# Kernel tuning notes

Hardware: AMD Instinct MI355X
Metric: run time of the kernel (lower is better)

## Reference

```python
import jax, jax.numpy as jnp
import numpy as np

# --- Mamba2Enc config (matches init_kwargs + mamba_ssm Mamba2 defaults) ---
D_IN = 1024
D_MODEL = 512
N_CLASSES = 2
NLAYERS = 2
D_STATE = 64
D_CONV = 4
EXPAND = 2
HEADDIM = 64
D_INNER = EXPAND * D_MODEL            # 1024
NHEADS = D_INNER // HEADDIM           # 16
CONV_DIM = D_INNER + 2 * D_STATE      # 1152 (ngroups=1)
D_IN_PROJ = 2 * D_INNER + 2 * D_STATE + NHEADS  # 2192
EPS = 1e-5


def setup_inputs() -> dict:
    key = jax.random.key(0)
    ks = jax.random.split(key, 10)
    def w(k, shape, sc=0.02):
        return jax.random.normal(k, shape, jnp.float32) * sc
    x = jax.random.normal(ks[0], (4, 4096, D_IN), jnp.float32)
    # fc1
    W1 = w(ks[1], (D_MODEL, D_IN))
    b1 = jnp.zeros((D_MODEL,), jnp.float32)
    # per-layer params stacked on leading NLAYERS axis
    ln_w = jnp.ones((NLAYERS, D_MODEL), jnp.float32)
    ln_b = jnp.zeros((NLAYERS, D_MODEL), jnp.float32)
    W_in = w(ks[2], (NLAYERS, D_IN_PROJ, D_MODEL))
    conv_w = w(ks[3], (NLAYERS, CONV_DIM, D_CONV), 0.1)
    conv_b = jnp.zeros((NLAYERS, CONV_DIM), jnp.float32)
    # dt_bias so that softplus(dt_bias) ~ [0.001, 0.1] (mamba init range)
    dt_bias = jax.random.uniform(ks[4], (NLAYERS, NHEADS), jnp.float32, -6.0, -2.3)
    A_log = jnp.log(jnp.tile(jnp.arange(1, NHEADS + 1, dtype=jnp.float32), (NLAYERS, 1)))
    Dskip = jnp.ones((NLAYERS, NHEADS), jnp.float32)
    norm_w = jnp.ones((NLAYERS, D_INNER), jnp.float32)
    W_out = w(ks[5], (NLAYERS, D_MODEL, D_INNER))
    # classifier
    Wc = w(ks[6], (N_CLASSES, D_MODEL))
    bc = jnp.zeros((N_CLASSES,), jnp.float32)
    return dict(x=x, W1=W1, b1=b1, ln_w=ln_w, ln_b=ln_b, W_in=W_in,
                conv_w=conv_w, conv_b=conv_b, dt_bias=dt_bias, A_log=A_log,
                Dskip=Dskip, norm_w=norm_w, W_out=W_out, Wc=Wc, bc=bc)


def _layernorm(h, w, b):
    mu = jnp.mean(h, axis=-1, keepdims=True)
    var = jnp.mean(jnp.square(h - mu), axis=-1, keepdims=True)
    return (h - mu) * jax.lax.rsqrt(var + EPS) * w + b


def _silu(x):
    return x * jax.nn.sigmoid(x)


def _mamba2(x, W_in, conv_w, conv_b, dt_bias, A_log, Dskip, norm_w, W_out):
    b, l, _ = x.shape
    zxbcdt = jnp.einsum('bld,ed->ble', x, W_in)  # (b, l, D_IN_PROJ)
    z = zxbcdt[..., :D_INNER]
    xBC = zxbcdt[..., D_INNER:D_INNER + CONV_DIM]
    dt = jax.nn.softplus(zxbcdt[..., -NHEADS:] + dt_bias)  # (b, l, h)
    # causal depthwise conv1d (kernel D_CONV) + silu
    xp = jnp.pad(xBC, ((0, 0), (D_CONV - 1, 0), (0, 0)))
    xBC = sum(xp[:, k:k + l, :] * conv_w[:, k] for k in range(D_CONV)) + conv_b
    xBC = _silu(xBC)
    xh = xBC[..., :D_INNER].reshape(b, l, NHEADS, HEADDIM)
    B = xBC[..., D_INNER:D_INNER + D_STATE]   # (b, l, n) ngroups=1
    C = xBC[..., D_INNER + D_STATE:]          # (b, l, n)
    A = -jnp.exp(A_log)                       # (h,)
    dA = jnp.exp(dt * A)                      # (b, l, h)
    dtx = dt[..., None] * xh                  # (b, l, h, p)

    def step(hstate, inp):
        dA_t, dtx_t, B_t, C_t = inp  # (b,h), (b,h,p), (b,n), (b,n)
        hstate = hstate * dA_t[:, :, None, None] + dtx_t[:, :, None, :] * B_t[:, None, :, None]
        y = jnp.einsum('bn,bhnp->bhp', C_t, hstate)
        return hstate, y

    init = jnp.zeros((b, NHEADS, D_STATE, HEADDIM), x.dtype)
    xs = (dA.transpose(1, 0, 2), dtx.transpose(1, 0, 2, 3),
          B.transpose(1, 0, 2), C.transpose(1, 0, 2))
    _, ys = jax.lax.scan(step, init, xs)      # ys: (l, b, h, p)
    y = ys.transpose(1, 0, 2, 3) + Dskip[None, None, :, None] * xh
    y = y.reshape(b, l, D_INNER)
    # RMSNormGated (norm_before_gate=False): rmsnorm(y * silu(z)) * weight
    y = y * _silu(z)
    y = y * jax.lax.rsqrt(jnp.mean(jnp.square(y), axis=-1, keepdims=True) + EPS) * norm_w
    return jnp.einsum('ble,de->bld', y, W_out)


def reference(x, W1, b1, ln_w, ln_b, W_in, conv_w, conv_b, dt_bias, A_log,
              Dskip, norm_w, W_out, Wc, bc):
    # fc1: Linear + GELU (dropout is identity at eval)
    h = jax.nn.gelu(jnp.einsum('bli,di->bld', x, W1) + b1, approximate=False)
    for i in range(NLAYERS):
        h = h + _mamba2(_layernorm(h, ln_w[i], ln_b[i]), W_in[i], conv_w[i],
                        conv_b[i], dt_bias[i], A_log[i], Dskip[i], norm_w[i], W_out[i])
    return jnp.einsum('bld,cd->blc', h, Wc) + bc
```

## Files before the change

kernel.cpp:

```cpp
#include <hip/hip_runtime.h>
#include <hip/hip_bf16.h>
#include <math.h>

#define BATCH 4
#define SEQ 4096
#define ROWS 16384
#define DIN 1024
#define DMODEL 512
#define DINNER 1024
#define DSTATE 64
#define NH 16
#define HD 64
#define CONVDIM 1152
#define DPROJ 2192
#define NPAD 2304
#define QC 64
#define NCH 64
#define LD 72

typedef __attribute__((ext_vector_type(8))) __bf16 bf16x8;
typedef __attribute__((ext_vector_type(4))) __bf16 bf16x4;
typedef __attribute__((ext_vector_type(4))) float f32x4;

__device__ __forceinline__ float siluf(float x){ return x / (1.f + __expf(-x)); }
__device__ __forceinline__ float geluf(float x){ return 0.5f*x*(1.f + erff(x*0.70710678118654752440f)); }

__device__ __forceinline__ bf16x8 scale8(bf16x8 v, float s){
  bf16x8 r;
  #pragma unroll
  for (int e = 0; e < 8; e++) r[e] = (__bf16)((float)v[e]*s);
  return r;
}

__device__ __forceinline__ void gl_lds16(const void* g, void* l){
  __builtin_amdgcn_global_load_lds((const __attribute__((address_space(1))) void*)g,
                                   (__attribute__((address_space(3))) void*)l, 16, 0, 0);
}

__global__ void cast_bf16_kernel(const float* __restrict__ src, __bf16* __restrict__ dst, long n){
  long i = (long)blockIdx.x*blockDim.x + threadIdx.x;
  long stride = (long)gridDim.x*blockDim.x;
  for (; i < n; i += stride) dst[i] = (__bf16)src[i];
}

__global__ void pad_win_kernel(const float* __restrict__ src, __bf16* __restrict__ dst){
  long total = 2L*NPAD*DMODEL;
  long i = (long)blockIdx.x*blockDim.x + threadIdx.x;
  long stride = (long)gridDim.x*blockDim.x;
  for (; i < total; i += stride){
    int k = (int)(i % DMODEL);
    int n = (int)((i / DMODEL) % NPAD);
    int l = (int)(i / ((long)DMODEL*NPAD));
    float v = (n < DPROJ) ? src[((long)l*DPROJ + n)*DMODEL + k] : 0.f;
    dst[i] = (__bf16)v;
  }
}

template<typename OutT, int EPI, int BM, int BN>
__global__ __launch_bounds__(256) void gemm_bt(const __bf16* __restrict__ A, const __bf16* __restrict__ Bm,
                                               OutT* __restrict__ C, const float* __restrict__ bias,
                                               int K, int Nc){
  constexpr int MI = BM/32, NI = BN/32;
  constexpr int CHA = BM/64;
  constexpr int CHT = (BM+BN)/64;
  __shared__ __align__(16) __bf16 As[2][BM*32];
  __shared__ __align__(16) __bf16 Bs[2][BN*32];
  int bm = blockIdx.x, bn = blockIdx.y;
  int tid = threadIdx.x;
  int lane = tid & 63, wid = tid >> 6;
  int wm = (wid >> 1)*(BM/2), wn = (wid & 1)*(BN/2);
  int lr = lane & 15, kb = lane >> 4;
  f32x4 acc[MI][NI] = {};
  const char* Ab = (const char*)A + (size_t)bm*BM*(size_t)(K*2);
  const char* Bb = (const char*)Bm + (size_t)bn*BN*(size_t)(K*2);
  int nkk = K >> 5;

  auto STAGE = [&](int kk, int buf){
    #pragma unroll
    for (int it = 0; it < CHT; it++){
      int cbase = it*4096 + wid*1024;
      int off = cbase + lane*16;
      int row = off >> 6, cb = off & 63;
      if (it < CHA) gl_lds16(Ab + (size_t)row*(K*2) + kk*64 + cb, (char*)(&As[buf][0]) + cbase);
      else          gl_lds16(Bb + (size_t)(row - BM)*(K*2) + kk*64 + cb, (char*)(&Bs[buf][0]) + (cbase - BM*64));
    }
  };

  STAGE(0, 0);
  for (int kk = 0; kk < nkk; kk++){
    int cur = kk & 1;
    if (kk + 1 < nkk){
      STAGE(kk + 1, cur ^ 1);
      asm volatile("s_waitcnt vmcnt(%0)" :: "n"(CHT) : "memory");
    } else {
      asm volatile("s_waitcnt vmcnt(0)" ::: "memory");
    }
    __builtin_amdgcn_sched_barrier(0);
    __builtin_amdgcn_s_barrier();
    __builtin_amdgcn_sched_barrier(0);
    const __bf16* Asb = &As[cur][0];
    const __bf16* Bsb = &Bs[cur][0];
    bf16x8 af[MI], bfr[NI];
    #pragma unroll
    for (int mi = 0; mi < MI; mi++) af[mi] = *(const bf16x8*)(Asb + (wm + mi*16 + lr)*32 + kb*8);
    #pragma unroll
    for (int ni = 0; ni < NI; ni++) bfr[ni] = *(const bf16x8*)(Bsb + (wn + ni*16 + lr)*32 + kb*8);
    #pragma unroll
    for (int mi = 0; mi < MI; mi++)
      #pragma unroll
      for (int ni = 0; ni < NI; ni++)
        acc[mi][ni] = __builtin_amdgcn_mfma_f32_16x16x32_bf16(af[mi], bfr[ni], acc[mi][ni], 0, 0, 0);
    __builtin_amdgcn_s_barrier();
    __builtin_amdgcn_sched_barrier(0);
  }
  #pragma unroll
  for (int mi = 0; mi < MI; mi++){
    #pragma unroll
    for (int ni = 0; ni < NI; ni++){
      int r0 = bm*BM + wm + mi*16 + (lane >> 4)*4;
      int c  = bn*BN + wn + ni*16 + lr;
      if (c < Nc){
        OutT* Cp = C + (size_t)r0*Nc + c;
        #pragma unroll
        for (int j = 0; j < 4; j++){
          float v = acc[mi][ni][j];
          if (EPI == 1){ float u = v + bias[c]; v = geluf(u); }
          if (EPI == 2){ v += (float)Cp[(size_t)j*Nc]; }
          Cp[(size_t)j*Nc] = (OutT)v;
        }
      }
    }
  }
}

__global__ __launch_bounds__(256) void ln_kernel(const float* __restrict__ h, const float* __restrict__ w,
                                                 const float* __restrict__ b, __bf16* __restrict__ out){
  int row = blockIdx.x*4 + (threadIdx.x >> 6);
  int lane = threadIdx.x & 63;
  const float* hr = h + (size_t)row*DMODEL + lane*8;
  float4 a = *(const float4*)hr, a2 = *(const float4*)(hr+4);
  float v[8] = {a.x,a.y,a.z,a.w,a2.x,a2.y,a2.z,a2.w};
  float s = 0.f;
  #pragma unroll
  for (int i = 0; i < 8; i++) s += v[i];
  #pragma unroll
  for (int o = 32; o; o >>= 1) s += __shfl_xor(s, o, 64);
  float mu = s*(1.f/512.f);
  float q = 0.f;
  #pragma unroll
  for (int i = 0; i < 8; i++){ float d = v[i]-mu; q += d*d; }
  #pragma unroll
  for (int o = 32; o; o >>= 1) q += __shfl_xor(q, o, 64);
  float rs = rsqrtf(q*(1.f/512.f) + 1e-5f);
  const float* wp = w + lane*8; const float* bp = b + lane*8;
  bf16x8 o8;
  #pragma unroll
  for (int i = 0; i < 8; i++) o8[i] = (__bf16)((v[i]-mu)*rs*wp[i] + bp[i]);
  *(bf16x8*)(out + (size_t)row*DMODEL + lane*8) = o8;
}

__global__ __launch_bounds__(256) void conv_bc(const __bf16* __restrict__ zx, const float* __restrict__ cw,
                                               const float* __restrict__ cb, __bf16* __restrict__ BCc){
  int idx = blockIdx.x*256 + threadIdx.x;
  int j = idx & 127;
  long bt = idx >> 7;
  int t = (int)(bt & (SEQ-1));
  int ch = DINNER + j;
  const __bf16* src = zx + (size_t)bt*DPROJ + 2048 + j;
  float acc = cb[ch] + (float)src[0]*cw[ch*4+3];
  if (t >= 1) acc += (float)src[-1L*DPROJ]*cw[ch*4+2];
  if (t >= 2) acc += (float)src[-2L*DPROJ]*cw[ch*4+1];
  if (t >= 3) acc += (float)src[-3L*DPROJ]*cw[ch*4+0];
  BCc[idx] = (__bf16)siluf(acc);
}

__global__ __launch_bounds__(256) void dt_kernel(const __bf16* __restrict__ zx, const float* __restrict__ dt_bias,
                                                 float* __restrict__ dtT){
  int idx = blockIdx.x*256 + threadIdx.x;
  int hh = idx & (NH-1); long bt = idx >> 4;
  int b = (int)(bt >> 12); int t = (int)(bt & (SEQ-1));
  float v = (float)zx[(size_t)bt*DPROJ + (DPROJ-NH) + hh] + dt_bias[hh];
  float sp = (v > 20.f) ? v : log1pf(__expf(v));
  dtT[((size_t)b*NH + hh)*SEQ + t] = sp;
}

__global__ __launch_bounds__(128) void ssd_state(const __bf16* __restrict__ zx, const __bf16* __restrict__ BCc,
                                                 const float* __restrict__ dtT, const float* __restrict__ A_log,
                                                 const float* __restrict__ cw, const float* __restrict__ cb,
                                                 __bf16* __restrict__ Schunk, float* __restrict__ Pbuf,
                                                 __bf16* __restrict__ xhT){
  __shared__ __align__(16) __bf16 Bt_all[2][64*LD];
  __shared__ __align__(16) __bf16 Xt_all[2][64*LD];
  int widx = threadIdx.x >> 6, lane = threadIdx.x & 63;
  int c = blockIdx.x*2 + widx, h = blockIdx.y, b = blockIdx.z;
  __bf16* Bt = Bt_all[widx];
  __bf16* Xt = Xt_all[widx];
  int lr = lane & 15, kb = lane >> 4, hi4 = lane >> 4;
  long t0 = (long)c*QC;
  size_t bt0 = (size_t)b*SEQ + t0;
  int bh = b*NH + h;
  float Ac = -expf(A_log[h]);
  float dtv = dtT[(size_t)bh*SEQ + t0 + lane];
  float cum = dtv*Ac;
  #pragma unroll
  for (int off = 1; off < 64; off <<= 1){ float v = __shfl_up(cum, off, 64); if (lane >= off) cum += v; }
  float cumQ = __shfl(cum, 63, 64);
  float w = __expf(cumQ - cum) * dtv;
  {
    const __bf16* bp = BCc + bt0*128 + lane;
    for (int tb = 0; tb < 8; tb++){
      bf16x8 buf;
      #pragma unroll
      for (int u = 0; u < 8; u++){
        int t = tb*8 + u;
        float bv = (float)bp[(size_t)t*128];
        buf[u] = (__bf16)(bv * __shfl(w, t, 64));
      }
      *(bf16x8*)&Bt[lane*LD + tb*8] = buf;
    }
  }
  {
    int ch = h*HD + lane;
    float w0 = cw[ch*4], w1 = cw[ch*4+1], w2 = cw[ch*4+2], w3 = cw[ch*4+3], cbv = cb[ch];
    const __bf16* xp = zx + bt0*DPROJ + (DINNER + ch);
    float x1 = (t0 >= 1) ? (float)xp[-1L*DPROJ] : 0.f;
    float x2 = (t0 >= 2) ? (float)xp[-2L*DPROJ] : 0.f;
    float x3 = (t0 >= 3) ? (float)xp[-3L*DPROJ] : 0.f;
    __bf16* xo = xhT + ((size_t)bh*NCH + c)*4096 + lane*64;
    for (int tb = 0; tb < 8; tb++){
      bf16x8 buf;
      #pragma unroll
      for (int u = 0; u < 8; u++){
        int t = tb*8 + u;
        float x0 = (float)xp[(size_t)t*DPROJ];
        float xv = siluf(cbv + w3*x0 + w2*x1 + w1*x2 + w0*x3);
        x3 = x2; x2 = x1; x1 = x0;
        buf[u] = (__bf16)xv;
      }
      *(bf16x8*)&Xt[lane*LD + tb*8] = buf;
      *(bf16x8*)(xo + tb*8) = buf;
    }
  }
  f32x4 acc[4][4] = {};
  #pragma unroll
  for (int kk = 0; kk < 2; kk++){
    bf16x8 af[4], bfr[4];
    #pragma unroll
    for (int mi = 0; mi < 4; mi++) af[mi]  = *(bf16x8*)&Bt[(mi*16+lr)*LD + kk*32 + kb*8];
    #pragma unroll
    for (int ni = 0; ni < 4; ni++) bfr[ni] = *(bf16x8*)&Xt[(ni*16+lr)*LD + kk*32 + kb*8];
    #pragma unroll
    for (int mi = 0; mi < 4; mi++)
      #pragma unroll
      for (int ni = 0; ni < 4; ni++)
        acc[mi][ni] = __builtin_amdgcn_mfma_f32_16x16x32_bf16(af[mi], bfr[ni], acc[mi][ni], 0, 0, 0);
  }
  __bf16* Sp = Schunk + ((size_t)bh*NCH + c)*4096;
  #pragma unroll
  for (int mi = 0; mi < 4; mi++)
    #pragma unroll
    for (int ni = 0; ni < 4; ni++){
      int n0 = mi*16 + hi4*4;
      int p  = ni*16 + lr;
      bf16x4 v;
      #pragma unroll
      for (int r = 0; r < 4; r++) v[r] = (__bf16)acc[mi][ni][r];
      *(bf16x4*)&Sp[p*64 + n0] = v;
    }
  if (lane == 0) Pbuf[bh*NCH + c] = __expf(cumQ);
}

__global__ __launch_bounds__(64) void ssd_comb(__bf16* __restrict__ Schunk, const float* __restrict__ Pbuf){
  int bh = blockIdx.x >> 4;
  int eb = blockIdx.x & 15;
  int e = eb*256 + threadIdx.x*4;
  __bf16* base = Schunk + (size_t)bh*NCH*4096 + e;
  float T0 = 0.f, T1 = 0.f, T2 = 0.f, T3 = 0.f;
  for (int c = 0; c < NCH; c++){
    float P = Pbuf[bh*NCH + c];
    bf16x4* p = (bf16x4*)(base + (size_t)c*4096);
    bf16x4 s = *p;
    bf16x4 o; o[0] = (__bf16)T0; o[1] = (__bf16)T1; o[2] = (__bf16)T2; o[3] = (__bf16)T3;
    *p = o;
    T0 = T0*P + (float)s[0]; T1 = T1*P + (float)s[1];
    T2 = T2*P + (float)s[2]; T3 = T3*P + (float)s[3];
  }
}

__global__ __launch_bounds__(256) void ssd_y(const __bf16* __restrict__ BCc, const float* __restrict__ dtT,
                                             const float* __restrict__ A_log, const float* __restrict__ Dskip,
                                             const __bf16* __restrict__ xhT, const __bf16* __restrict__ Spre,
                                             __bf16* __restrict__ yout){
  __shared__ __align__(16) __bf16 Gs_all[4][64*LD];
  __shared__ float cum_all[4][64], dt_all[4][64];
  int widx = threadIdx.x >> 6, lane = threadIdx.x & 63;
  int c = blockIdx.x*4 + widx, h = blockIdx.y, b = blockIdx.z;
  __bf16* Gs = Gs_all[widx];
  float* cum_s = cum_all[widx];
  float* dt_s = dt_all[widx];
  int lr = lane & 15, kb = lane >> 4, hi4 = lane >> 4;
  long t0 = (long)c*QC;
  size_t bt0 = (size_t)b*SEQ + t0;
  int bh = b*NH + h;
  float Ac = -expf(A_log[h]);
  float Dk = Dskip[h];
  float dtv = dtT[(size_t)bh*SEQ + t0 + lane];
  float cum = dtv*Ac;
  #pragma unroll
  for (int off = 1; off < 64; off <<= 1){ float v = __shfl_up(cum, off, 64); if (lane >= off) cum += v; }
  cum_s[lane] = cum; dt_s[lane] = dtv;
  bf16x8 cf[4][2];
  #pragma unroll
  for (int ni = 0; ni < 4; ni++)
    #pragma unroll
    for (int kk = 0; kk < 2; kk++)
      cf[ni][kk] = *(const bf16x8*)&BCc[(bt0 + ni*16 + lr)*128 + 64 + kk*32 + kb*8];
  f32x4 g[4][4] = {};
  #pragma unroll
  for (int kk = 0; kk < 2; kk++){
    bf16x8 bfj[4];
    #pragma unroll
    for (int mi = 0; mi < 4; mi++) bfj[mi] = *(const bf16x8*)&BCc[(bt0 + mi*16 + lr)*128 + kk*32 + kb*8];
    #pragma unroll
    for (int mi = 0; mi < 4; mi++)
      #pragma unroll
      for (int ni = 0; ni < 4; ni++)
        g[mi][ni] = __builtin_amdgcn_mfma_f32_16x16x32_bf16(bfj[mi], cf[ni][kk], g[mi][ni], 0, 0, 0);
  }
  float cumi[4];
  #pragma unroll
  for (int ni = 0; ni < 4; ni++) cumi[ni] = cum_s[ni*16 + lr];
  #pragma unroll
  for (int mi = 0; mi < 4; mi++){
    #pragma unroll
    for (int r = 0; r < 4; r++){
      int j = mi*16 + hi4*4 + r;
      float cj = cum_s[j], dj = dt_s[j];
      #pragma unroll
      for (int ni = 0; ni < 4; ni++){
        int i = ni*16 + lr;
        float v = g[mi][ni][r];
        if (i > j)       v = v * __expf(cumi[ni] - cj) * dj;
        else if (i == j) v = v*dj + Dk;
        else             v = 0.f;
        g[mi][ni][r] = v;
      }
    }
  }
  #pragma unroll
  for (int mi = 0; mi < 4; mi++)
    #pragma unroll
    for (int ni = 0; ni < 4; ni++){
      int j0 = mi*16 + hi4*4;
      int i  = ni*16 + lr;
      bf16x4 v;
      #pragma unroll
      for (int r = 0; r < 4; r++) v[r] = (__bf16)g[mi][ni][r];
      *(bf16x4*)&Gs[i*LD + j0] = v;
    }
  const __bf16* Xp = xhT + ((size_t)bh*NCH + c)*4096;
  f32x4 y4[4][4] = {};
  #pragma unroll
  for (int kk = 0; kk < 2; kk++){
    bf16x8 af2[4], bf2[4];
    #pragma unroll
    for (int mi = 0; mi < 4; mi++) af2[mi] = *(const bf16x8*)&Xp[(mi*16+lr)*64 + kk*32 + kb*8];
    #pragma unroll
    for (int ni = 0; ni < 4; ni++) bf2[ni] = *(bf16x8*)&Gs[(ni*16+lr)*LD + kk*32 + kb*8];
    #pragma unroll
    for (int mi = 0; mi < 4; mi++)
      #pragma unroll
      for (int ni = 0; ni < 4; ni++)
        y4[mi][ni] = __builtin_amdgcn_mfma_f32_16x16x32_bf16(af2[mi], bf2[ni], y4[mi][ni], 0, 0, 0);
  }
  {
    const __bf16* Sp = Spre + ((size_t)bh*NCH + c)*4096;
    float ei[4];
    #pragma unroll
    for (int ni = 0; ni < 4; ni++) ei[ni] = __expf(cumi[ni]);
    #pragma unroll
    for (int kk = 0; kk < 2; kk++){
      bf16x8 as1[4];
      #pragma unroll
      for (int mi = 0; mi < 4; mi++) as1[mi] = *(const bf16x8*)&Sp[(mi*16+lr)*64 + kk*32 + kb*8];
      #pragma unroll
      for (int ni = 0; ni < 4; ni++){
        bf16x8 cs = scale8(cf[ni][kk], ei[ni]);
        #pragma unroll
        for (int mi = 0; mi < 4; mi++)
          y4[mi][ni] = __builtin_amdgcn_mfma_f32_16x16x32_bf16(as1[mi], cs, y4[mi][ni], 0, 0, 0);
      }
    }
  }
  #pragma unroll
  for (int mi = 0; mi < 4; mi++)
    #pragma unroll
    for (int ni = 0; ni < 4; ni++){
      int p0 = mi*16 + hi4*4;
      int i  = ni*16 + lr;
      bf16x4 v;
      #pragma unroll
      for (int r = 0; r < 4; r++) v[r] = (__bf16)y4[mi][ni][r];
      *(bf16x4*)&yout[(bt0 + i)*DINNER + h*HD + p0] = v;
    }
}

__global__ __launch_bounds__(256) void gate_rms(__bf16* __restrict__ y, const __bf16* __restrict__ zx,
                                                const float* __restrict__ nw){
  int row = blockIdx.x*4 + (threadIdx.x >> 6);
  int lane = threadIdx.x & 63;
  __bf16* yr = y + (size_t)row*DINNER + lane*16;
  const __bf16* zr = zx + (size_t)row*DPROJ + lane*16;
  bf16x8 y0 = *(const bf16x8*)yr, y1 = *(const bf16x8*)(yr+8);
  bf16x8 z0 = *(const bf16x8*)zr, z1 = *(const bf16x8*)(zr+8);
  float v[16]; float ss = 0.f;
  #pragma unroll
  for (int i = 0; i < 8; i++){ float z = (float)z0[i]; float tv = (float)y0[i]*siluf(z); v[i] = tv; ss += tv*tv; }
  #pragma unroll
  for (int i = 0; i < 8; i++){ float z = (float)z1[i]; float tv = (float)y1[i]*siluf(z); v[8+i] = tv; ss += tv*tv; }
  #pragma unroll
  for (int o = 32; o; o >>= 1) ss += __shfl_xor(ss, o, 64);
  float rs = rsqrtf(ss*(1.f/1024.f) + 1e-5f);
  const float* np = nw + lane*16;
  bf16x8 o0, o1;
  #pragma unroll
  for (int i = 0; i < 8; i++){ o0[i] = (__bf16)(v[i]*rs*np[i]); o1[i] = (__bf16)(v[8+i]*rs*np[8+i]); }
  *(bf16x8*)yr = o0; *(bf16x8*)(yr+8) = o1;
}

__global__ __launch_bounds__(256) void cls_kernel(const float* __restrict__ h, const float* __restrict__ Wc,
                                                  const float* __restrict__ bc, float* __restrict__ out){
  int row = blockIdx.x*4 + (threadIdx.x >> 6);
  int lane = threadIdx.x & 63;
  const float* hr = h + (size_t)row*DMODEL + lane*8;
  float4 a = *(const float4*)hr, a2 = *(const float4*)(hr+4);
  float hv[8] = {a.x,a.y,a.z,a.w,a2.x,a2.y,a2.z,a2.w};
  const float* w0 = Wc + lane*8;
  const float* w1 = Wc + DMODEL + lane*8;
  float s0 = 0.f, s1 = 0.f;
  #pragma unroll
  for (int i = 0; i < 8; i++){ s0 += hv[i]*w0[i]; s1 += hv[i]*w1[i]; }
  #pragma unroll
  for (int o = 32; o; o >>= 1){ s0 += __shfl_xor(s0, o, 64); s1 += __shfl_xor(s1, o, 64); }
  if (lane == 0){ out[(size_t)row*2] = s0 + bc[0]; out[(size_t)row*2 + 1] = s1 + bc[1]; }
}

extern "C" void kernel_launch(void* const* d_in, const int* in_sizes, int n_in,
                              void* d_out, int out_size, void* d_ws, size_t ws_size,
                              hipStream_t stream){
  const float* x       = (const float*)d_in[0];
  const float* W1      = (const float*)d_in[1];
  const float* b1      = (const float*)d_in[2];
  const float* ln_w    = (const float*)d_in[3];
  const float* ln_b    = (const float*)d_in[4];
  const float* W_in    = (const float*)d_in[5];
  const float* conv_w  = (const float*)d_in[6];
  const float* conv_b  = (const float*)d_in[7];
  const float* dt_bias = (const float*)d_in[8];
  const float* A_log   = (const float*)d_in[9];
  const float* Dskip   = (const float*)d_in[10];
  const float* norm_w  = (const float*)d_in[11];
  const float* W_out   = (const float*)d_in[12];
  const float* Wc      = (const float*)d_in[13];
  const float* bc      = (const float*)d_in[14];
  float* out = (float*)d_out;
  char* ws = (char*)d_ws;

  size_t off = 0;
  auto alloc = [&](size_t bytes){ void* p = ws + off; off += (bytes + 255) & ~(size_t)255; return p; };
  char*   regionA = (char*) alloc((size_t)ROWS*DIN*2);
  __bf16* W1b     = (__bf16*)alloc((size_t)DMODEL*DIN*2);
  __bf16* Winb    = (__bf16*)alloc(2L*NPAD*DMODEL*2);
  __bf16* Woutb   = (__bf16*)alloc(2L*DMODEL*DINNER*2);
  float*  h       = (float*) alloc((size_t)ROWS*DMODEL*4);
  __bf16* zx      = (__bf16*)alloc((size_t)ROWS*DPROJ*2);
  __bf16* BCc     = (__bf16*)alloc((size_t)ROWS*128*2);
  float*  dtT     = (float*) alloc((size_t)ROWS*NH*4);
  __bf16* ybuf    = (__bf16*)alloc((size_t)ROWS*DINNER*2);
  __bf16* xhT     = (__bf16*)alloc((size_t)ROWS*DINNER*2);
  float*  Pbuf    = (float*) alloc(64L*NCH*4);
  if (off > ws_size) return;

  __bf16* x_bf   = (__bf16*)regionA;
  __bf16* hnb    = (__bf16*)regionA;
  __bf16* Schunk = (__bf16*)regionA;

  cast_bf16_kernel<<<4096, 256, 0, stream>>>(x, x_bf, (long)ROWS*DIN);
  cast_bf16_kernel<<<512, 256, 0, stream>>>(W1, W1b, (long)DMODEL*DIN);
  cast_bf16_kernel<<<1024, 256, 0, stream>>>(W_out, Woutb, 2L*DMODEL*DINNER);
  pad_win_kernel<<<2048, 256, 0, stream>>>(W_in, Winb);

  {
    dim3 g(ROWS/64, DMODEL/128);
    gemm_bt<float,1,64,128><<<g, 256, 0, stream>>>(x_bf, W1b, h, b1, DIN, DMODEL);
  }

  for (int l = 0; l < 2; l++){
    ln_kernel<<<ROWS/4, 256, 0, stream>>>(h, ln_w + l*DMODEL, ln_b + l*DMODEL, hnb);
    {
      dim3 g(ROWS/128, NPAD/128);
      gemm_bt<__bf16,0,128,128><<<g, 256, 0, stream>>>(hnb, Winb + (size_t)l*NPAD*DMODEL, zx, nullptr, DMODEL, DPROJ);
    }
    conv_bc<<<(ROWS*128)/256, 256, 0, stream>>>(zx, conv_w + l*CONVDIM*4, conv_b + l*CONVDIM, BCc);
    dt_kernel<<<(ROWS*NH)/256, 256, 0, stream>>>(zx, dt_bias + l*NH, dtT);
    {
      dim3 gs(NCH/2, NH, BATCH);
      ssd_state<<<gs, 128, 0, stream>>>(zx, BCc, dtT, A_log + l*NH,
                                        conv_w + l*CONVDIM*4, conv_b + l*CONVDIM, Schunk, Pbuf, xhT);
      ssd_comb<<<64*16, 64, 0, stream>>>(Schunk, Pbuf);
      dim3 gy(NCH/4, NH, BATCH);
      ssd_y<<<gy, 256, 0, stream>>>(BCc, dtT, A_log + l*NH, Dskip + l*NH, xhT, Schunk, ybuf);
    }
    gate_rms<<<ROWS/4, 256, 0, stream>>>(ybuf, zx, norm_w + l*DINNER);
    {
      dim3 g(ROWS/64, DMODEL/128);
      gemm_bt<float,2,64,128><<<g, 256, 0, stream>>>(ybuf, Woutb + (size_t)l*DMODEL*DINNER, h, nullptr, DINNER, DMODEL);
    }
  }

  cls_kernel<<<ROWS/4, 256, 0, stream>>>(h, Wc, bc, out);
}
```

Before: 496.8 us.

## Triple-buffer GEMM LDS staging and store residual stream in bf16

The GEMM now uses three LDS buffers and prefetches two K-steps ahead, with vmcnt waits adjusted to match, to better hide global load latency. Separately, the residual stream h is stored as bf16 instead of fp32, which halves traffic for the layernorm, residual-add epilogue and classifier reads. The cost is more LDS per block, which may reduce occupancy, and lower precision in the accumulated residual across layers.

```diff
diff --git a/kernel.cpp b/kernel.cpp
--- a/kernel.cpp
+++ b/kernel.cpp
@@ -63,8 +63,8 @@
   constexpr int MI = BM/32, NI = BN/32;
   constexpr int CHA = BM/64;
   constexpr int CHT = (BM+BN)/64;
-  __shared__ __align__(16) __bf16 As[2][BM*32];
-  __shared__ __align__(16) __bf16 Bs[2][BN*32];
+  __shared__ __align__(16) __bf16 As[3][BM*32];
+  __shared__ __align__(16) __bf16 Bs[3][BN*32];
   int bm = blockIdx.x, bn = blockIdx.y;
   int tid = threadIdx.x;
   int lane = tid & 63, wid = tid >> 6;
@@ -87,10 +87,13 @@
   };
 
   STAGE(0, 0);
+  if (nkk > 1) STAGE(1, 1);
   for (int kk = 0; kk < nkk; kk++){
-    int cur = kk & 1;
-    if (kk + 1 < nkk){
-      STAGE(kk + 1, cur ^ 1);
+    int cur = kk % 3;
+    if (kk + 2 < nkk){
+      STAGE(kk + 2, (kk + 2) % 3);
+      asm volatile("s_waitcnt vmcnt(%0)" :: "n"(2*CHT) : "memory");
+    } else if (kk + 1 < nkk){
       asm volatile("s_waitcnt vmcnt(%0)" :: "n"(CHT) : "memory");
     } else {
       asm volatile("s_waitcnt vmcnt(0)" ::: "memory");
@@ -133,13 +136,15 @@
   }
 }
 
-__global__ __launch_bounds__(256) void ln_kernel(const float* __restrict__ h, const float* __restrict__ w,
+__global__ __launch_bounds__(256) void ln_kernel(const __bf16* __restrict__ h, const float* __restrict__ w,
                                                  const float* __restrict__ b, __bf16* __restrict__ out){
   int row = blockIdx.x*4 + (threadIdx.x >> 6);
   int lane = threadIdx.x & 63;
-  const float* hr = h + (size_t)row*DMODEL + lane*8;
-  float4 a = *(const float4*)hr, a2 = *(const float4*)(hr+4);
-  float v[8] = {a.x,a.y,a.z,a.w,a2.x,a2.y,a2.z,a2.w};
+  const __bf16* hr = h + (size_t)row*DMODEL + lane*8;
+  bf16x8 a = *(const bf16x8*)hr;
+  float v[8];
+  #pragma unroll
+  for (int i = 0; i < 8; i++) v[i] = (float)a[i];
   float s = 0.f;
   #pragma unroll
   for (int i = 0; i < 8; i++) s += v[i];
@@ -428,13 +433,15 @@
   *(bf16x8*)yr = o0; *(bf16x8*)(yr+8) = o1;
 }
 
-__global__ __launch_bounds__(256) void cls_kernel(const float* __restrict__ h, const float* __restrict__ Wc,
+__global__ __launch_bounds__(256) void cls_kernel(const __bf16* __restrict__ h, const float* __restrict__ Wc,
                                                   const float* __restrict__ bc, float* __restrict__ out){
   int row = blockIdx.x*4 + (threadIdx.x >> 6);
   int lane = threadIdx.x & 63;
-  const float* hr = h + (size_t)row*DMODEL + lane*8;
-  float4 a = *(const float4*)hr, a2 = *(const float4*)(hr+4);
-  float hv[8] = {a.x,a.y,a.z,a.w,a2.x,a2.y,a2.z,a2.w};
+  const __bf16* hr = h + (size_t)row*DMODEL + lane*8;
+  bf16x8 a = *(const bf16x8*)hr;
+  float hv[8];
+  #pragma unroll
+  for (int i = 0; i < 8; i++) hv[i] = (float)a[i];
   const float* w0 = Wc + lane*8;
   const float* w1 = Wc + DMODEL + lane*8;
   float s0 = 0.f, s1 = 0.f;
@@ -472,7 +479,7 @@
   __bf16* W1b     = (__bf16*)alloc((size_t)DMODEL*DIN*2);
   __bf16* Winb    = (__bf16*)alloc(2L*NPAD*DMODEL*2);
   __bf16* Woutb   = (__bf16*)alloc(2L*DMODEL*DINNER*2);
-  float*  h       = (float*) alloc((size_t)ROWS*DMODEL*4);
+  __bf16* h       = (__bf16*)alloc((size_t)ROWS*DMODEL*2);
   __bf16* zx      = (__bf16*)alloc((size_t)ROWS*DPROJ*2);
   __bf16* BCc     = (__bf16*)alloc((size_t)ROWS*128*2);
   float*  dtT     = (float*) alloc((size_t)ROWS*NH*4);
@@ -492,7 +499,7 @@
 
   {
     dim3 g(ROWS/64, DMODEL/128);
-    gemm_bt<float,1,64,128><<<g, 256, 0, stream>>>(x_bf, W1b, h, b1, DIN, DMODEL);
+    gemm_bt<__bf16,1,64,128><<<g, 256, 0, stream>>>(x_bf, W1b, h, b1, DIN, DMODEL);
   }
 
   for (int l = 0; l < 2; l++){
@@ -514,7 +521,7 @@
     gate_rms<<<ROWS/4, 256, 0, stream>>>(ybuf, zx, norm_w + l*DINNER);
     {
       dim3 g(ROWS/64, DMODEL/128);
-      gemm_bt<float,2,64,128><<<g, 256, 0, stream>>>(ybuf, Woutb + (size_t)l*DMODEL*DINNER, h, nullptr, DINNER, DMODEL);
+      gemm_bt<__bf16,2,64,128><<<g, 256, 0, stream>>>(ybuf, Woutb + (size_t)l*DMODEL*DINNER, h, nullptr, DINNER, DMODEL);
     }
   }
 
```

Measured after the change: 488.2 us. Within noise of the previous version (-1.7%).
